# Optimization experiments

Measured on AMD Instinct MI355X. Metric: run time of the kernel, lower is better.

Reference implementation:

```python
import jax, jax.numpy as jnp
import numpy as np

INPUT_DIM = 64
HIDDEN_DIM = 512
DIM_INNER = int(HIDDEN_DIM * 1.5)  # 768


def log_g(x):
    # torch.where(x >= 0, (relu(x) + 0.5).log(), -softplus(-x))
    return jnp.where(x >= 0, jnp.log(jax.nn.relu(x) + 0.5), -jax.nn.softplus(-x))


def setup_inputs() -> dict:
    key = jax.random.key(0)
    k_x, k1, k2, k3, k4 = jax.random.split(key, 5)
    B, S = 16, 4096
    x = jax.random.normal(k_x, (B, S, INPUT_DIM), dtype=jnp.float32)
    # weights stored as [in, out] (transpose of torch Linear.weight); bias=False everywhere
    W_in = jax.random.normal(k1, (INPUT_DIM, HIDDEN_DIM), dtype=jnp.float32) * 0.02
    W_hg = jax.random.normal(k2, (HIDDEN_DIM, 2 * DIM_INNER), dtype=jnp.float32) * 0.02
    W_out = jax.random.normal(k3, (DIM_INNER, HIDDEN_DIM), dtype=jnp.float32) * 0.02
    W_final = jax.random.normal(k4, (HIDDEN_DIM, 1), dtype=jnp.float32) * 0.02
    return {"x": x, "W_in": W_in, "W_hg": W_hg, "W_out": W_out, "W_final": W_final}


def reference(x, W_in, W_hg, W_out, W_final):
    # x: [B, S, input_dim]
    h = jnp.einsum('bsi,ih->bsh', x, W_in)                 # [B,S,H]
    hg = jnp.einsum('bsh,hd->bsd', h, W_hg)                # [B,S,2*DI]
    hidden, gate = jnp.split(hg, 2, axis=-1)               # each [B,S,DI]
    # seq_len > 1 path, prev_hidden=None
    log_coeffs = -jax.nn.softplus(gate)                    # log(1 - z)
    log_z = -jax.nn.softplus(-gate)                        # log(z)
    log_values = log_z + log_g(hidden)
    # heinsen associative scan in log space
    a_star = jnp.cumsum(log_coeffs, axis=1)
    log_h = a_star + jax.lax.cumlogsumexp(log_values - a_star, axis=1)
    out = jnp.exp(log_h)                                   # [B,S,DI]
    out = jnp.einsum('bsd,dh->bsh', out, W_out)            # [B,S,H]
    predictions = jnp.einsum('bsh,ho->bso', out, W_final)[..., 0]  # [B,S]
    return predictions
```

## Files before the change

### kernel.cpp

```cpp
#include <hip/hip_runtime.h>
#include <hip/hip_fp16.h>

typedef unsigned short u16;
typedef unsigned int   u32;
typedef __bf16 bf16x8 __attribute__((ext_vector_type(8)));
typedef float  f32x4  __attribute__((ext_vector_type(4)));

constexpr int BB   = 16;
constexpr int S    = 4096;
constexpr int M    = BB * S;
constexpr int DIN  = 64;
constexpr int H    = 512;
constexpr int DI   = 768;
constexpr int N2   = 1536;
constexpr int CL   = 128;
constexpr int NCHB = S / CL;
constexpr int NCHUNK = M / CL;
constexpr int DTILES = 12;

constexpr size_t OFF_XB   = 0;
constexpr size_t OFF_B2C  = 8388608;
constexpr size_t OFF_WC   = 8585216;
constexpr size_t OFF_CC   = 8589312;
constexpr size_t OFF_HE   = OFF_CC  + 1572864;
constexpr size_t OFF_HIN  = OFF_HE  + 1572864;
constexpr size_t OFF_PART = OFF_HIN + 1572864;

constexpr float L2E = 1.4426950408889634f;

__device__ __forceinline__ u16 f2bf(float f) {
  u32 u = __float_as_uint(f);
  u32 r = (u + 0x7FFFu + ((u >> 16) & 1u)) >> 16;
  return (u16)r;
}

__device__ __forceinline__ int cvs(int row, int d) {
  return row * 64 + (d ^ (((row >> 2) & 3) << 4));
}

__global__ __launch_bounds__(256) void prep_xb(const float* __restrict__ x,
                                               u16* __restrict__ xb) {
  size_t i = (size_t)(blockIdx.x * 256 + threadIdx.x) * 8;
  float4 f0 = *(const float4*)(x + i);
  float4 f1 = *(const float4*)(x + i + 4);
  u32 w0 = f2bf(f0.x) | ((u32)f2bf(f0.y) << 16);
  u32 w1 = f2bf(f0.z) | ((u32)f2bf(f0.w) << 16);
  u32 w2 = f2bf(f1.x) | ((u32)f2bf(f1.y) << 16);
  u32 w3 = f2bf(f1.z) | ((u32)f2bf(f1.w) << 16);
  uint4 o = make_uint4(w0, w1, w2, w3);
  *(uint4*)(xb + i) = o;
}

__global__ __launch_bounds__(256) void prep_b2c(const float* __restrict__ Win,
                                                const float* __restrict__ Whg,
                                                u16* __restrict__ B2c) {
  __shared__ float Wl[64][65];
  const int tid = threadIdx.x;
  const int k = tid & 63;
  const int nloc = tid >> 6;
  const int n = blockIdx.x * 4 + nloc;
  const int g = n >> 5, r = n & 31;
  const int col = (r < 16) ? (g * 16 + r) : (DI + g * 16 + (r - 16));
  float acc = 0.f;
  for (int jc = 0; jc < H; jc += 64) {
    const int jl = tid & 63, k0 = tid >> 6;
    #pragma unroll
    for (int s = 0; s < 16; ++s) {
      int kr = k0 + 4 * s;
      Wl[kr][jl] = Win[kr * H + jc + jl];
    }
    __syncthreads();
    #pragma unroll 8
    for (int j = 0; j < 64; ++j)
      acc = fmaf(Wl[k][j], Whg[(size_t)(jc + j) * N2 + col], acc);
    __syncthreads();
  }
  B2c[n * 64 + k] = f2bf(acc);
}

__global__ __launch_bounds__(256) void prep_wcomb(const float* __restrict__ Wout,
                                                  const float* __restrict__ Wfin,
                                                  float* __restrict__ wc) {
  int wv = threadIdx.x >> 6, ln = threadIdx.x & 63;
  int d = blockIdx.x * 4 + wv;
  const float* row = Wout + (size_t)d * H;
  float s = 0.f;
  #pragma unroll
  for (int j = 0; j < 8; ++j) {
    int k = j * 64 + ln;
    s += row[k] * Wfin[k];
  }
  #pragma unroll
  for (int off = 32; off; off >>= 1) s += __shfl_xor(s, off);
  if (ln == 0) wc[d] = s;
}

template<int PASS>
__global__ __launch_bounds__(256) void fused_gemm_scan(
    const u16* __restrict__ xb, const u16* __restrict__ B2c,
    const float* __restrict__ Hin, const float* __restrict__ wcomb,
    float* __restrict__ Cc, float* __restrict__ He,
    float* __restrict__ part) {
  __shared__ __align__(16) u16 AB[16384];
  __shared__ float SC[4][64], SV[4][64];
  u32* cvl = (u32*)AB;

  const int tid = threadIdx.x, wv = tid >> 6, ln = tid & 63;
  const int nt = blockIdx.x % DTILES, ck = blockIdx.x / DTILES;
  const int m0 = ck * CL;
  const int wr = wv >> 1, wcol = wv & 1;
  const int lrow = ln & 15, lk = (ln >> 4) * 8;

  {
    const uint4* gA = (const uint4*)(xb + (size_t)m0 * 64);
    const uint4* gB = (const uint4*)(B2c + (size_t)nt * 128 * 64);
    uint4* lA = (uint4*)AB;
    uint4* lB = (uint4*)(AB + 8192);
    #pragma unroll
    for (int j = 0; j < 4; ++j) {
      int q = j * 256 + tid;
      lA[q] = gA[q];
      lB[q] = gB[q];
    }
  }
  __syncthreads();

  f32x4 acc[4][4] = {};
  {
    const u16* Al = AB;
    const u16* Bl = AB + 8192;
    #pragma unroll
    for (int kk = 0; kk < 2; ++kk) {
      bf16x8 af[4], bfr[4];
      #pragma unroll
      for (int i = 0; i < 4; ++i)
        af[i] = *(const bf16x8*)&Al[(wr * 64 + i * 16 + lrow) * 64 + kk * 32 + lk];
      #pragma unroll
      for (int j = 0; j < 4; ++j)
        bfr[j] = *(const bf16x8*)&Bl[(wcol * 64 + j * 16 + lrow) * 64 + kk * 32 + lk];
      #pragma unroll
      for (int i = 0; i < 4; ++i)
        #pragma unroll
        for (int j = 0; j < 4; ++j)
          acc[i][j] = __builtin_amdgcn_mfma_f32_16x16x32_bf16(af[i], bfr[j], acc[i][j], 0, 0, 0);
    }
  }
  __syncthreads();

  #pragma unroll
  for (int i = 0; i < 4; ++i)
    #pragma unroll
    for (int jp = 0; jp < 2; ++jp) {
      f32x4 hid = acc[i][2 * jp + 0];
      f32x4 gat = acc[i][2 * jp + 1];
      const int dl = (wcol * 2 + jp) * 16 + lrow;
      #pragma unroll
      for (int r = 0; r < 4; ++r) {
        int row = wr * 64 + i * 16 + (ln >> 4) * 4 + r;
        float gate = gat[r], hidden = hid[r];
        float eg  = __builtin_amdgcn_exp2f(gate * L2E);
        float cc  = __builtin_amdgcn_rcpf(1.0f + eg);
        float zz  = eg * cc;
        float gneg = __builtin_amdgcn_rcpf(
                        1.0f + __builtin_amdgcn_exp2f(-hidden * L2E));
        float gg  = (hidden >= 0.0f) ? (hidden + 0.5f) : gneg;
        float vv  = zz * gg;
        __half2 p = __floats2half2_rn(cc, vv);
        cvl[cvs(row, dl)] = *(const u32*)&p;
      }
    }
  __syncthreads();

  float Cp = 1.f, Vp = 0.f;
  #pragma unroll 8
  for (int tt = 0; tt < 32; ++tt) {
    u32 u = cvl[cvs(wv * 32 + tt, ln)];
    __half2 hv = *(const __half2*)&u;
    float2 f = __half22float2(hv);
    Vp = fmaf(f.x, Vp, f.y);
    Cp *= f.x;
  }
  SC[wv][ln] = Cp;
  SV[wv][ln] = Vp;
  __syncthreads();

  if (PASS == 1) {
    if (wv == 0) {
      float C = SC[0][ln], V = SV[0][ln];
      #pragma unroll
      for (int s = 1; s < 4; ++s) {
        V = fmaf(SC[s][ln], V, SV[s][ln]);
        C *= SC[s][ln];
      }
      int idx = ck * DI + nt * 64 + ln;
      Cc[idx] = C;
      He[idx] = V;
    }
  } else {
    float h = Hin[ck * DI + nt * 64 + ln];
    if (wv >= 1) h = fmaf(SC[0][ln], h, SV[0][ln]);
    if (wv >= 2) h = fmaf(SC[1][ln], h, SV[1][ln]);
    if (wv >= 3) h = fmaf(SC[2][ln], h, SV[2][ln]);
    const float wd = wcomb[nt * 64 + ln];
    #pragma unroll 4
    for (int tt = 0; tt < 32; ++tt) {
      const int t = wv * 32 + tt;
      u32 u = cvl[cvs(t, ln)];
      __half2 hv = *(const __half2*)&u;
      float2 f = __half22float2(hv);
      h = fmaf(f.x, h, f.y);
      float pv = h * wd;
      cvl[t * 64 + ((ln + t) & 63)] = __float_as_uint(pv);
    }
    __syncthreads();
    const int row = tid >> 1, half = tid & 1;
    float s = 0.f;
    #pragma unroll 8
    for (int jj = 0; jj < 32; ++jj) {
      int idx = (half * 32 + jj + row) & 63;
      s += __uint_as_float(cvl[row * 64 + idx]);
    }
    s += __shfl_xor(s, 1);
    if (half == 0) part[(size_t)nt * M + m0 + row] = s;
  }
}

__global__ __launch_bounds__(768) void scan_carry(const float* __restrict__ Cc,
                                                  const float* __restrict__ He,
                                                  float* __restrict__ Hin) {
  const int b = blockIdx.x, d = threadIdx.x;
  float carry = 0.f;
  for (int q = 0; q < NCHB; ++q) {
    int idx = (b * NCHB + q) * DI + d;
    Hin[idx] = carry;
    carry = fmaf(Cc[idx], carry, He[idx]);
  }
}

__global__ __launch_bounds__(256) void reduce12(const float* __restrict__ part,
                                                float* __restrict__ out) {
  int i = blockIdx.x * 256 + threadIdx.x;
  float s = 0.f;
  #pragma unroll
  for (int w = 0; w < DTILES; ++w) s += part[(size_t)w * M + i];
  out[i] = s;
}

extern "C" void kernel_launch(void* const* d_in, const int* in_sizes, int n_in,
                              void* d_out, int out_size, void* d_ws, size_t ws_size,
                              hipStream_t stream) {
  const float* x    = (const float*)d_in[0];
  const float* Win  = (const float*)d_in[1];
  const float* Whg  = (const float*)d_in[2];
  const float* Wout = (const float*)d_in[3];
  const float* Wfin = (const float*)d_in[4];
  float* out = (float*)d_out;
  char* ws = (char*)d_ws;

  u16*   xb   = (u16*)(ws + OFF_XB);
  u16*   B2c  = (u16*)(ws + OFF_B2C);
  float* wc   = (float*)(ws + OFF_WC);
  float* Cc   = (float*)(ws + OFF_CC);
  float* He   = (float*)(ws + OFF_HE);
  float* Hin  = (float*)(ws + OFF_HIN);
  float* part = (float*)(ws + OFF_PART);

  prep_xb   <<<2048, 256, 0, stream>>>(x, xb);
  prep_b2c  <<<384,  256, 0, stream>>>(Win, Whg, B2c);
  prep_wcomb<<<192,  256, 0, stream>>>(Wout, Wfin, wc);
  fused_gemm_scan<1><<<NCHUNK * DTILES, 256, 0, stream>>>(xb, B2c, Hin, wc, Cc, He, part);
  scan_carry<<<BB, DI, 0, stream>>>(Cc, He, Hin);
  fused_gemm_scan<2><<<NCHUNK * DTILES, 256, 0, stream>>>(xb, B2c, Hin, wc, Cc, He, part);
  reduce12  <<<256,  256, 0, stream>>>(part, out);
}
```

Measured before the change: 149.9 us.

## Write per-wave scan segments and swizzle LDS tiles to avoid bank conflicts

Each wave now writes its own 32-row segment carry (product and value) to global memory, replacing the in-block cross-wave combine through shared memory. This removes a barrier and the extra serial pass in pass 2. The carry scan kernel handles four times as many segments sequentially and updates the value buffer in place. The LDS layout for the A/B GEMM tiles is also XOR-swizzled to reduce bank conflicts on MFMA fragment loads. The cost is more global traffic and a longer serial carry scan (128 steps per batch instead of 32).

```diff
diff --git a/kernel.cpp b/kernel.cpp
--- a/kernel.cpp
+++ b/kernel.cpp
@@ -14,17 +14,17 @@
 constexpr int DI   = 768;
 constexpr int N2   = 1536;
 constexpr int CL   = 128;
-constexpr int NCHB = S / CL;
 constexpr int NCHUNK = M / CL;
+constexpr int NSEG  = NCHUNK * 4;
+constexpr int SEGB  = S / 32;
 constexpr int DTILES = 12;
 
-constexpr size_t OFF_XB   = 0;
-constexpr size_t OFF_B2C  = 8388608;
-constexpr size_t OFF_WC   = 8585216;
-constexpr size_t OFF_CC   = 8589312;
-constexpr size_t OFF_HE   = OFF_CC  + 1572864;
-constexpr size_t OFF_HIN  = OFF_HE  + 1572864;
-constexpr size_t OFF_PART = OFF_HIN + 1572864;
+constexpr size_t OFF_XB    = 0;
+constexpr size_t OFF_B2C   = 8388608;
+constexpr size_t OFF_WC    = 8585216;
+constexpr size_t OFF_SEGC  = 8589312;
+constexpr size_t OFF_SEGVH = 14880768;
+constexpr size_t OFF_PART  = 21172224;
 
 constexpr float L2E = 1.4426950408889634f;
 
@@ -99,17 +99,16 @@
 __global__ __launch_bounds__(256) void fused_gemm_scan(
     const u16* __restrict__ xb, const u16* __restrict__ B2c,
     const float* __restrict__ Hin, const float* __restrict__ wcomb,
-    float* __restrict__ Cc, float* __restrict__ He,
+    float* __restrict__ SegC, float* __restrict__ SegV,
     float* __restrict__ part) {
   __shared__ __align__(16) u16 AB[16384];
-  __shared__ float SC[4][64], SV[4][64];
   u32* cvl = (u32*)AB;
 
   const int tid = threadIdx.x, wv = tid >> 6, ln = tid & 63;
   const int nt = blockIdx.x % DTILES, ck = blockIdx.x / DTILES;
   const int m0 = ck * CL;
   const int wr = wv >> 1, wcol = wv & 1;
-  const int lrow = ln & 15, lk = (ln >> 4) * 8;
+  const int lrow = ln & 15, hi4 = ln >> 4;
 
   {
     const uint4* gA = (const uint4*)(xb + (size_t)m0 * 64);
@@ -119,8 +118,9 @@
     #pragma unroll
     for (int j = 0; j < 4; ++j) {
       int q = j * 256 + tid;
-      lA[q] = gA[q];
-      lB[q] = gB[q];
+      int qs = (q & ~7) | ((q & 7) ^ ((q >> 3) & 7));
+      lA[qs] = gA[q];
+      lB[qs] = gB[q];
     }
   }
   __syncthreads();
@@ -133,11 +133,15 @@
     for (int kk = 0; kk < 2; ++kk) {
       bf16x8 af[4], bfr[4];
       #pragma unroll
-      for (int i = 0; i < 4; ++i)
-        af[i] = *(const bf16x8*)&Al[(wr * 64 + i * 16 + lrow) * 64 + kk * 32 + lk];
-      #pragma unroll
-      for (int j = 0; j < 4; ++j)
-        bfr[j] = *(const bf16x8*)&Bl[(wcol * 64 + j * 16 + lrow) * 64 + kk * 32 + lk];
+      for (int i = 0; i < 4; ++i) {
+        int row = wr * 64 + i * 16 + lrow;
+        af[i] = *(const bf16x8*)&Al[row * 64 + (((kk * 4 + hi4) ^ (row & 7)) << 3)];
+      }
+      #pragma unroll
+      for (int j = 0; j < 4; ++j) {
+        int row = wcol * 64 + j * 16 + lrow;
+        bfr[j] = *(const bf16x8*)&Bl[row * 64 + (((kk * 4 + hi4) ^ (row & 7)) << 3)];
+      }
       #pragma unroll
       for (int i = 0; i < 4; ++i)
         #pragma unroll
@@ -156,7 +160,7 @@
       const int dl = (wcol * 2 + jp) * 16 + lrow;
       #pragma unroll
       for (int r = 0; r < 4; ++r) {
-        int row = wr * 64 + i * 16 + (ln >> 4) * 4 + r;
+        int row = wr * 64 + i * 16 + hi4 * 4 + r;
         float gate = gat[r], hidden = hid[r];
         float eg  = __builtin_amdgcn_exp2f(gate * L2E);
         float cc  = __builtin_amdgcn_rcpf(1.0f + eg);
@@ -171,44 +175,31 @@
     }
   __syncthreads();
 
-  float Cp = 1.f, Vp = 0.f;
-  #pragma unroll 8
-  for (int tt = 0; tt < 32; ++tt) {
-    u32 u = cvl[cvs(wv * 32 + tt, ln)];
-    __half2 hv = *(const __half2*)&u;
-    float2 f = __half22float2(hv);
-    Vp = fmaf(f.x, Vp, f.y);
-    Cp *= f.x;
-  }
-  SC[wv][ln] = Cp;
-  SV[wv][ln] = Vp;
-  __syncthreads();
-
+  const int seg = ck * 4 + wv;
   if (PASS == 1) {
-    if (wv == 0) {
-      float C = SC[0][ln], V = SV[0][ln];
-      #pragma unroll
-      for (int s = 1; s < 4; ++s) {
-        V = fmaf(SC[s][ln], V, SV[s][ln]);
-        C *= SC[s][ln];
-      }
-      int idx = ck * DI + nt * 64 + ln;
-      Cc[idx] = C;
-      He[idx] = V;
-    }
+    float Cp = 1.f, Vp = 0.f;
+    #pragma unroll 8
+    for (int tt = 0; tt < 32; ++tt) {
+      u32 u = cvl[cvs(wv * 32 + tt, ln)];
+      __half2 hv = *(const __half2*)&u;
+      float c = __half2float(__low2half(hv));
+      float v = __half2float(__high2half(hv));
+      Vp = fmaf(c, Vp, v);
+      Cp *= c;
+    }
+    SegC[(size_t)seg * DI + nt * 64 + ln] = Cp;
+    SegV[(size_t)seg * DI + nt * 64 + ln] = Vp;
   } else {
-    float h = Hin[ck * DI + nt * 64 + ln];
-    if (wv >= 1) h = fmaf(SC[0][ln], h, SV[0][ln]);
-    if (wv >= 2) h = fmaf(SC[1][ln], h, SV[1][ln]);
-    if (wv >= 3) h = fmaf(SC[2][ln], h, SV[2][ln]);
+    float h = Hin[(size_t)seg * DI + nt * 64 + ln];
     const float wd = wcomb[nt * 64 + ln];
     #pragma unroll 4
     for (int tt = 0; tt < 32; ++tt) {
       const int t = wv * 32 + tt;
       u32 u = cvl[cvs(t, ln)];
       __half2 hv = *(const __half2*)&u;
-      float2 f = __half22float2(hv);
-      h = fmaf(f.x, h, f.y);
+      float c = __half2float(__low2half(hv));
+      float v = __half2float(__high2half(hv));
+      h = fmaf(c, h, v);
       float pv = h * wd;
       cvl[t * 64 + ((ln + t) & 63)] = __float_as_uint(pv);
     }
@@ -225,15 +216,15 @@
   }
 }
 
-__global__ __launch_bounds__(768) void scan_carry(const float* __restrict__ Cc,
-                                                  const float* __restrict__ He,
-                                                  float* __restrict__ Hin) {
+__global__ __launch_bounds__(768) void scan_carry(const float* __restrict__ SegC,
+                                                  float* __restrict__ SegVH) {
   const int b = blockIdx.x, d = threadIdx.x;
   float carry = 0.f;
-  for (int q = 0; q < NCHB; ++q) {
-    int idx = (b * NCHB + q) * DI + d;
-    Hin[idx] = carry;
-    carry = fmaf(Cc[idx], carry, He[idx]);
+  for (int q = 0; q < SEGB; ++q) {
+    size_t idx = (size_t)(b * SEGB + q) * DI + d;
+    float tmp = fmaf(SegC[idx], carry, SegVH[idx]);
+    SegVH[idx] = carry;
+    carry = tmp;
   }
 }
 
@@ -257,19 +248,18 @@
   float* out = (float*)d_out;
   char* ws = (char*)d_ws;
 
-  u16*   xb   = (u16*)(ws + OFF_XB);
-  u16*   B2c  = (u16*)(ws + OFF_B2C);
-  float* wc   = (float*)(ws + OFF_WC);
-  float* Cc   = (float*)(ws + OFF_CC);
-  float* He   = (float*)(ws + OFF_HE);
-  float* Hin  = (float*)(ws + OFF_HIN);
-  float* part = (float*)(ws + OFF_PART);
+  u16*   xb    = (u16*)(ws + OFF_XB);
+  u16*   B2c   = (u16*)(ws + OFF_B2C);
+  float* wc    = (float*)(ws + OFF_WC);
+  float* SegC  = (float*)(ws + OFF_SEGC);
+  float* SegVH = (float*)(ws + OFF_SEGVH);
+  float* part  = (float*)(ws + OFF_PART);
 
   prep_xb   <<<2048, 256, 0, stream>>>(x, xb);
   prep_b2c  <<<384,  256, 0, stream>>>(Win, Whg, B2c);
   prep_wcomb<<<192,  256, 0, stream>>>(Wout, Wfin, wc);
-  fused_gemm_scan<1><<<NCHUNK * DTILES, 256, 0, stream>>>(xb, B2c, Hin, wc, Cc, He, part);
-  scan_carry<<<BB, DI, 0, stream>>>(Cc, He, Hin);
-  fused_gemm_scan<2><<<NCHUNK * DTILES, 256, 0, stream>>>(xb, B2c, Hin, wc, Cc, He, part);
+  fused_gemm_scan<1><<<NCHUNK * DTILES, 256, 0, stream>>>(xb, B2c, SegVH, wc, SegC, SegVH, part);
+  scan_carry<<<BB, DI, 0, stream>>>(SegC, SegVH);
+  fused_gemm_scan<2><<<NCHUNK * DTILES, 256, 0, stream>>>(xb, B2c, SegVH, wc, SegC, SegVH, part);
   reduce12  <<<256,  256, 0, stream>>>(part, out);
 }
```

Measured after the change: 151.6 us. Within noise of the previous version (+1.1%).
